# Optimization experiments

Hardware: AMD Instinct MI355X
Metric: run time of the kernel (lower is better)

The kernel has to match this reference:

```python
import jax, jax.numpy as jnp
import numpy as np

N_NODES = 100000
N_EDGES = 800000
N_GRAPHS = 128
UNITS = 128
NUM_GINS = 3
NUM_CLASSES = 16
EPS_GIN = 0.5        # GIN eps from the module
BN_EPS = 1e-3        # keras BatchNormalization default epsilon


def setup_inputs() -> dict:
    key = jax.random.key(0)
    ks = jax.random.split(key, 12)
    x = jax.random.normal(ks[0], (N_NODES, UNITS), dtype=jnp.float32)
    edge_index = jax.random.randint(ks[1], (2, N_EDGES), 0, N_NODES, dtype=jnp.int32)
    edge_weight = jax.random.uniform(ks[2], (N_EDGES,), dtype=jnp.float32)
    node_graph_index = jnp.sort(jax.random.randint(ks[3], (N_NODES,), 0, N_GRAPHS, dtype=jnp.int32))
    s1 = 1.0 / np.sqrt(UNITS)
    W1 = jax.random.normal(ks[4], (NUM_GINS, UNITS, UNITS), dtype=jnp.float32) * s1
    b1 = jnp.zeros((NUM_GINS, UNITS), jnp.float32)
    W2 = jax.random.normal(ks[5], (NUM_GINS, UNITS, UNITS), dtype=jnp.float32) * s1
    b2 = jnp.zeros((NUM_GINS, UNITS), jnp.float32)
    gamma = jnp.ones((NUM_GINS, UNITS), jnp.float32)
    beta = jnp.zeros((NUM_GINS, UNITS), jnp.float32)
    bn_mean = jnp.zeros((NUM_GINS, UNITS), jnp.float32)
    bn_var = jnp.ones((NUM_GINS, UNITS), jnp.float32)
    Wm1 = jax.random.normal(ks[6], (NUM_GINS * UNITS, 128), dtype=jnp.float32) / np.sqrt(NUM_GINS * UNITS)
    bm1 = jnp.zeros((128,), jnp.float32)
    Wm2 = jax.random.normal(ks[7], (128, NUM_CLASSES), dtype=jnp.float32) / np.sqrt(128.0)
    bm2 = jnp.zeros((NUM_CLASSES,), jnp.float32)
    return dict(x=x, edge_index=edge_index, edge_weight=edge_weight,
                node_graph_index=node_graph_index,
                W1=W1, b1=b1, W2=W2, b2=b2, gamma=gamma, beta=beta,
                bn_mean=bn_mean, bn_var=bn_var,
                Wm1=Wm1, bm1=bm1, Wm2=Wm2, bm2=bm2)


def reference(x, edge_index, edge_weight, node_graph_index,
              W1, b1, W2, b2, gamma, beta, bn_mean, bn_var,
              Wm1, bm1, Wm2, bm2):
    dst, src = edge_index[0], edge_index[1]
    h = x
    hidden_outputs = []
    for i in range(NUM_GINS):
        # message passing: weighted neighbor sum (gather + scatter-add)
        msg = h[src] * edge_weight[:, None]                      # [E, U]
        agg = jax.ops.segment_sum(msg, dst, num_segments=N_NODES)  # [N, U]
        z = (1.0 + EPS_GIN) * h + agg
        # GIN MLP: Dense-relu, Dense, BatchNorm (inference), relu
        z = jax.nn.relu(z @ W1[i] + b1[i])
        z = z @ W2[i] + b2[i]
        z = (z - bn_mean[i]) * (gamma[i] / jnp.sqrt(bn_var[i] + BN_EPS)) + beta[i]
        h = jax.nn.relu(z)
        hidden_outputs.append(h)
    hcat = jnp.concatenate(hidden_outputs, axis=-1)              # [N, 3*U]
    pooled = jax.ops.segment_sum(hcat, node_graph_index, num_segments=N_GRAPHS)  # [G, 3*U]
    g = jax.nn.relu(pooled @ Wm1 + bm1)                          # dropout is identity at inference
    logits = g @ Wm2 + bm2
    return logits
```

## Files before the change

### kernel.cpp

```cpp
#include <hip/hip_runtime.h>

#define NN 100000
#define NE 800000
#define NG 128
#define U  128
#define NGIN 3
#define NBUCK 64
#define NPB 1563
#define ACHUNK 4096
#define NAB ((NE + ACHUNK - 1) / ACHUNK)
#define ZP 136

typedef short bf16x8 __attribute__((ext_vector_type(8)));
typedef float f32x4 __attribute__((ext_vector_type(4)));

__device__ __forceinline__ unsigned short f2b(float f) {
    union { float f; unsigned u; } v; v.f = f;
    unsigned r = v.u + 0x7FFF + ((v.u >> 16) & 1);
    return (unsigned short)(r >> 16);
}
__device__ __forceinline__ float blo(unsigned u) {
    union { unsigned u; float f; } v; v.u = u << 16; return v.f;
}
__device__ __forceinline__ float bhi(unsigned u) {
    union { unsigned u; float f; } v; v.u = u & 0xffff0000u; return v.f;
}
__device__ __forceinline__ unsigned cvtpk(float lo, float hi) {
    unsigned r;
    asm("v_cvt_pk_bf16_f32 %0, %1, %2" : "=v"(r) : "v"(lo), "v"(hi));
    return r;
}

__global__ __launch_bounds__(256) void convert_k(const float* __restrict__ x,
                                                 unsigned short* __restrict__ hb) {
    int i = blockIdx.x * 256 + threadIdx.x;
    if (i >= NN * U / 4) return;
    float4 v = reinterpret_cast<const float4*>(x)[i];
    uint2 o;
    o.x = (unsigned)f2b(v.x) | ((unsigned)f2b(v.y) << 16);
    o.y = (unsigned)f2b(v.z) | ((unsigned)f2b(v.w) << 16);
    reinterpret_cast<uint2*>(hb)[i] = o;
}

__global__ __launch_bounds__(256) void wfrag_k(const float* __restrict__ W1,
                                               const float* __restrict__ W2,
                                               unsigned short* __restrict__ wfrag) {
    int b = blockIdx.x;
    const float* src = ((b & 1) ? W2 : W1) + (size_t)(b >> 1) * U * U;
    unsigned short* dst = wfrag + (size_t)b * 16384;
    for (int e = threadIdx.x; e < 16384; e += 256) {
        int j = e & 7, lane = (e >> 3) & 63, ks = (e >> 9) & 3, ct = e >> 11;
        int k = ks * 32 + ((lane >> 4) << 3) + j;
        int c = ct * 16 + (lane & 15);
        dst[e] = f2b(src[k * U + c]);
    }
}

__global__ __launch_bounds__(128) void bnprep_k(const float* __restrict__ b2,
                                                const float* __restrict__ gam,
                                                const float* __restrict__ bet,
                                                const float* __restrict__ mean,
                                                const float* __restrict__ var,
                                                float* __restrict__ scl,
                                                float* __restrict__ sh) {
    int i = blockIdx.x * 128 + threadIdx.x;
    float s = gam[i] * rsqrtf(var[i] + 1e-3f);
    scl[i] = s;
    sh[i] = (b2[i] - mean[i]) * s + bet[i];
}

__global__ __launch_bounds__(256) void bhist_k(const int* __restrict__ ei,
                                               int* __restrict__ bcnt) {
    __shared__ int lh[NBUCK];
    int tid = threadIdx.x;
    if (tid < NBUCK) lh[tid] = 0;
    __syncthreads();
    int e0 = blockIdx.x * ACHUNK;
    int eend = min(e0 + ACHUNK, NE);
    for (int e = e0 + tid; e < eend; e += 256)
        atomicAdd(&lh[ei[e] / NPB], 1);
    __syncthreads();
    if (tid < NBUCK && lh[tid]) atomicAdd(&bcnt[tid], lh[tid]);
}

__global__ __launch_bounds__(64) void bscan_k(const int* __restrict__ bcnt,
                                              int* __restrict__ bcur,
                                              int* __restrict__ boff,
                                              int* __restrict__ rowptr) {
    int lane = threadIdx.x;
    int v = bcnt[lane];
    int incl = v;
#pragma unroll
    for (int off = 1; off < 64; off <<= 1) {
        int n = __shfl_up(incl, off);
        if (lane >= off) incl += n;
    }
    int excl = incl - v;
    bcur[lane] = excl;
    boff[lane] = excl;
    if (lane == 63) { boff[64] = incl; rowptr[NN] = NE; }
}

__global__ __launch_bounds__(256) void phaseA_k(const int* __restrict__ ei,
                                                const float* __restrict__ ew,
                                                int* __restrict__ bcur,
                                                uint2* __restrict__ tmp) {
    __shared__ int lh[NBUCK];
    int tid = threadIdx.x;
    if (tid < NBUCK) lh[tid] = 0;
    __syncthreads();
    int e0 = blockIdx.x * ACHUNK;
    int eend = min(e0 + ACHUNK, NE);
    for (int e = e0 + tid; e < eend; e += 256)
        atomicAdd(&lh[ei[e] / NPB], 1);
    __syncthreads();
    if (tid < NBUCK) {
        int c = lh[tid];
        lh[tid] = c ? atomicAdd(&bcur[tid], c) : 0;
    }
    __syncthreads();
    for (int e = e0 + tid; e < eend; e += 256) {
        int d = ei[e];
        int pos = atomicAdd(&lh[d / NPB], 1);
        uint2 r;
        r.x = ((unsigned)ei[NE + e] << 15) | (unsigned)f2b(ew[e]);
        r.y = (unsigned)d;
        tmp[pos] = r;
    }
}

__global__ __launch_bounds__(256) void phaseB_k(const uint2* __restrict__ tmp,
                                                const int* __restrict__ boff,
                                                int* __restrict__ rowptr,
                                                unsigned* __restrict__ esw) {
    __shared__ int cnt[1792];
    __shared__ int ws[4];
    const int tid = threadIdx.x;
    const int b = blockIdx.x;
    const int n0 = b * NPB;
    const int npb = min(NPB, NN - n0);
    const int wbeg = boff[b], wend = boff[b + 1];

    for (int i = tid; i < 1792; i += 256) cnt[i] = 0;
    __syncthreads();
    for (int e = wbeg + tid; e < wend; e += 256)
        atomicAdd(&cnt[(int)tmp[e].y - n0], 1);
    __syncthreads();
    int base = tid * 7;
    int v[7]; int s = 0;
#pragma unroll
    for (int k = 0; k < 7; ++k) { v[k] = cnt[base + k]; s += v[k]; }
    int lane = tid & 63, wid = tid >> 6;
    int incl = s;
#pragma unroll
    for (int off = 1; off < 64; off <<= 1) {
        int n = __shfl_up(incl, off);
        if (lane >= off) incl += n;
    }
    if (lane == 63) ws[wid] = incl;
    __syncthreads();
    if (tid == 0) {
        int a = 0;
#pragma unroll
        for (int w = 0; w < 4; ++w) { int t = ws[w]; ws[w] = a; a += t; }
    }
    __syncthreads();
    int run = wbeg + ws[wid] + (incl - s);
#pragma unroll
    for (int k = 0; k < 7; ++k) { cnt[base + k] = run; run += v[k]; }
    __syncthreads();
    for (int i = tid; i < npb; i += 256) rowptr[n0 + i] = cnt[i];
    __syncthreads();
    for (int e = wbeg + tid; e < wend; e += 256) {
        uint2 r = tmp[e];
        int pos = atomicAdd(&cnt[(int)r.y - n0], 1);
        esw[pos] = r.x;
    }
}

__global__ __launch_bounds__(256) void fusedgd_k(const unsigned short* __restrict__ hin,
                                                 const unsigned* __restrict__ esw,
                                                 const int* __restrict__ rowptr,
                                                 const unsigned short* __restrict__ wf1,
                                                 const unsigned short* __restrict__ wf2,
                                                 const float* __restrict__ bias1,
                                                 const float* __restrict__ sclp,
                                                 const float* __restrict__ shp,
                                                 const int* __restrict__ gidx,
                                                 unsigned short* __restrict__ hout,
                                                 float* __restrict__ pooled,
                                                 int pool_off) {
    __shared__ unsigned short zt[16 * ZP];
    __shared__ unsigned short z1t[16 * ZP];
    const int tid = threadIdx.x;
    const int lane = tid & 63;
    const int wid = tid >> 6;
    const int r0 = blockIdx.x * 16;
    const unsigned* hp = reinterpret_cast<const unsigned*>(hin);
    unsigned* ztd = reinterpret_cast<unsigned*>(zt);

    for (int q = 0; q < 4; ++q) {
        int row = wid * 4 + q;
        int node = r0 + row;
        int beg = rowptr[node], end = rowptr[node + 1];
        float ax[8], ay[8];
#pragma unroll
        for (int k = 0; k < 8; ++k) { ax[k] = 0.f; ay[k] = 0.f; }
        for (int cb = beg; cb < end; cb += 64) {
            int n = min(end - cb, 64);
            unsigned rec = (lane < n) ? esw[cb + lane] : 0u;
            int sv = (int)(rec >> 15);
            float wv = __uint_as_float((rec & 0x7FFFu) << 16);
            for (int i = 0; i < n; i += 8) {
                int s_[8]; float w_[8]; unsigned h_[8];
#pragma unroll
                for (int k = 0; k < 8; ++k) {
                    s_[k] = __shfl(sv, i + k);
                    w_[k] = __shfl(wv, i + k);
                }
#pragma unroll
                for (int k = 0; k < 8; ++k)
                    h_[k] = hp[(size_t)s_[k] * 64 + lane];
#pragma unroll
                for (int k = 0; k < 8; ++k) {
                    ax[k] = fmaf(blo(h_[k]), w_[k], ax[k]);
                    ay[k] = fmaf(bhi(h_[k]), w_[k], ay[k]);
                }
            }
        }
        float axs = ((ax[0] + ax[1]) + (ax[2] + ax[3])) + ((ax[4] + ax[5]) + (ax[6] + ax[7]));
        float ays = ((ay[0] + ay[1]) + (ay[2] + ay[3])) + ((ay[4] + ay[5]) + (ay[6] + ay[7]));
        unsigned hn = hp[(size_t)node * 64 + lane];
        axs = fmaf(1.5f, blo(hn), axs);
        ays = fmaf(1.5f, bhi(hn), ays);
        ztd[row * (ZP / 2) + lane] = cvtpk(axs, ays);
    }
    __syncthreads();

    const int c = lane & 15;
    const int g = lane >> 4;
    bf16x8 a1[4];
#pragma unroll
    for (int ks = 0; ks < 4; ++ks)
        a1[ks] = *reinterpret_cast<const bf16x8*>(zt + c * ZP + ks * 32 + g * 8);

    f32x4 acc1[2];
    acc1[0] = (f32x4){0.f, 0.f, 0.f, 0.f};
    acc1[1] = (f32x4){0.f, 0.f, 0.f, 0.f};
#pragma unroll
    for (int t = 0; t < 2; ++t) {
        int ct = wid * 2 + t;
#pragma unroll
        for (int ks = 0; ks < 4; ++ks) {
            bf16x8 b = *reinterpret_cast<const bf16x8*>(
                wf1 + (((ct * 4 + ks) * 64 + lane) << 3));
            acc1[t] = __builtin_amdgcn_mfma_f32_16x16x32_bf16(a1[ks], b, acc1[t], 0, 0, 0);
        }
    }
#pragma unroll
    for (int t = 0; t < 2; ++t) {
        int col = (wid * 2 + t) * 16 + c;
        float bv = bias1[col];
#pragma unroll
        for (int j = 0; j < 4; ++j) {
            int row = g * 4 + j;
            z1t[row * ZP + col] = f2b(fmaxf(acc1[t][j] + bv, 0.f));
        }
    }
    __syncthreads();

    bf16x8 a2[4];
#pragma unroll
    for (int ks = 0; ks < 4; ++ks)
        a2[ks] = *reinterpret_cast<const bf16x8*>(z1t + c * ZP + ks * 32 + g * 8);

    f32x4 acc2[2];
    acc2[0] = (f32x4){0.f, 0.f, 0.f, 0.f};
    acc2[1] = (f32x4){0.f, 0.f, 0.f, 0.f};
#pragma unroll
    for (int t = 0; t < 2; ++t) {
        int ct = wid * 2 + t;
#pragma unroll
        for (int ks = 0; ks < 4; ++ks) {
            bf16x8 b = *reinterpret_cast<const bf16x8*>(
                wf2 + (((ct * 4 + ks) * 64 + lane) << 3));
            acc2[t] = __builtin_amdgcn_mfma_f32_16x16x32_bf16(a2[ks], b, acc2[t], 0, 0, 0);
        }
    }

    int ga = gidx[r0], gb = gidx[r0 + 15];
    bool uni = (ga == gb);
#pragma unroll
    for (int t = 0; t < 2; ++t) {
        int col = (wid * 2 + t) * 16 + c;
        float scl = sclp[col], sh = shp[col];
        float hv[4];
        float psum = 0.f;
#pragma unroll
        for (int j = 0; j < 4; ++j) {
            int row = g * 4 + j;
            float v = fmaxf(fmaf(acc2[t][j], scl, sh), 0.f);
            hv[j] = v;
            psum += v;
            hout[(size_t)(r0 + row) * U + col] = f2b(v);
        }
        if (uni) {
            psum += __shfl_xor(psum, 16);
            psum += __shfl_xor(psum, 32);
            if (lane < 16)
                unsafeAtomicAdd(&pooled[(size_t)ga * (NGIN * U) + pool_off + col], psum);
        } else {
#pragma unroll
            for (int j = 0; j < 4; ++j)
                unsafeAtomicAdd(&pooled[(size_t)gidx[r0 + g * 4 + j] * (NGIN * U) + pool_off + col], hv[j]);
        }
    }
}

__global__ __launch_bounds__(128) void mlp1_k(const float* __restrict__ pooled,
                                              const float* __restrict__ Wm1,
                                              const float* __restrict__ bm1,
                                              float* __restrict__ g) {
    __shared__ float sp[NGIN * U];
    int gi = blockIdx.x, c = threadIdx.x;
    for (int j = c; j < NGIN * U; j += 128) sp[j] = pooled[(size_t)gi * (NGIN * U) + j];
    __syncthreads();
    float acc = bm1[c];
    for (int k = 0; k < NGIN * U; ++k) acc = fmaf(sp[k], Wm1[(size_t)k * 128 + c], acc);
    g[gi * 128 + c] = fmaxf(acc, 0.f);
}

__global__ __launch_bounds__(256) void mlp2_k(const float* __restrict__ g,
                                              const float* __restrict__ Wm2,
                                              const float* __restrict__ bm2,
                                              float* __restrict__ out) {
    int idx = blockIdx.x * 256 + threadIdx.x;
    int gi = idx >> 4, c = idx & 15;
    float acc = bm2[c];
    for (int k = 0; k < 128; ++k) acc = fmaf(g[gi * 128 + k], Wm2[k * 16 + c], acc);
    out[gi * 16 + c] = acc;
}

extern "C" void kernel_launch(void* const* d_in, const int* in_sizes, int n_in,
                              void* d_out, int out_size, void* d_ws, size_t ws_size,
                              hipStream_t stream) {
    const float* x   = (const float*)d_in[0];
    const int*   ei  = (const int*)d_in[1];
    const float* ew  = (const float*)d_in[2];
    const int*   gix = (const int*)d_in[3];
    const float* W1  = (const float*)d_in[4];
    const float* b1  = (const float*)d_in[5];
    const float* W2  = (const float*)d_in[6];
    const float* b2  = (const float*)d_in[7];
    const float* gam = (const float*)d_in[8];
    const float* bet = (const float*)d_in[9];
    const float* bmn = (const float*)d_in[10];
    const float* bvr = (const float*)d_in[11];
    const float* Wm1 = (const float*)d_in[12];
    const float* bm1 = (const float*)d_in[13];
    const float* Wm2 = (const float*)d_in[14];
    const float* bm2 = (const float*)d_in[15];
    float* out = (float*)d_out;

    unsigned short* hb0 = (unsigned short*)d_ws;
    unsigned short* hb1 = hb0 + (size_t)NN * U;
    float* pooled = (float*)(hb1 + (size_t)NN * U);
    float* gbuf   = pooled + (size_t)NG * (NGIN * U);
    unsigned short* wfrag = (unsigned short*)(gbuf + (size_t)NG * 128);
    unsigned* esw = (unsigned*)(wfrag + 6 * 16384);
    uint2* tmp    = (uint2*)(esw + NE);
    int*   rowptr = (int*)(tmp + NE);
    int*   bcnt   = rowptr + (NN + 1);
    int*   bcur   = bcnt + NBUCK;
    int*   boff   = bcur + NBUCK;
    float* sclp   = (float*)(boff + NBUCK + 1);
    float* shp    = sclp + NGIN * U;

    convert_k<<<(NN * U / 4 + 255) / 256, 256, 0, stream>>>(x, hb0);
    hipMemsetAsync(bcnt, 0, NBUCK * sizeof(int), stream);
    bhist_k<<<NAB, 256, 0, stream>>>(ei, bcnt);
    bscan_k<<<1, 64, 0, stream>>>(bcnt, bcur, boff, rowptr);
    phaseA_k<<<NAB, 256, 0, stream>>>(ei, ew, bcur, tmp);
    phaseB_k<<<NBUCK, 256, 0, stream>>>(tmp, boff, rowptr, esw);
    wfrag_k<<<6, 256, 0, stream>>>(W1, W2, wfrag);
    bnprep_k<<<NGIN, 128, 0, stream>>>(b2, gam, bet, bmn, bvr, sclp, shp);
    hipMemsetAsync(pooled, 0, (size_t)NG * (NGIN * U) * sizeof(float), stream);

    unsigned short* hA = hb0;
    unsigned short* hB = hb1;
    for (int i = 0; i < NGIN; ++i) {
        fusedgd_k<<<NN / 16, 256, 0, stream>>>(
            hA, esw, rowptr,
            wfrag + (size_t)(2 * i) * 16384, wfrag + (size_t)(2 * i + 1) * 16384,
            b1 + i * U, sclp + i * U, shp + i * U,
            gix, hB, pooled, i * U);
        unsigned short* t = hA; hA = hB; hB = t;
    }
    mlp1_k<<<NG, 128, 0, stream>>>(pooled, Wm1, bm1, gbuf);
    mlp2_k<<<(NG * 16) / 256, 256, 0, stream>>>(gbuf, Wm2, bm2, out);
}
```

Before: 288.1 us.

## Pad CSR rows to multiples of 8 and interleave four rows per warp gather

```diff
diff --git a/kernel.cpp b/kernel.cpp
--- a/kernel.cpp
+++ b/kernel.cpp
@@ -10,6 +10,7 @@
 #define ACHUNK 4096
 #define NAB ((NE + ACHUNK - 1) / ACHUNK)
 #define ZP 136
+#define ESWSZ (NE + 8 * NN + 64)
 
 typedef short bf16x8 __attribute__((ext_vector_type(8)));
 typedef float f32x4 __attribute__((ext_vector_type(4)));
@@ -85,8 +86,7 @@
 
 __global__ __launch_bounds__(64) void bscan_k(const int* __restrict__ bcnt,
                                               int* __restrict__ bcur,
-                                              int* __restrict__ boff,
-                                              int* __restrict__ rowptr) {
+                                              int* __restrict__ boff) {
     int lane = threadIdx.x;
     int v = bcnt[lane];
     int incl = v;
@@ -98,7 +98,7 @@
     int excl = incl - v;
     bcur[lane] = excl;
     boff[lane] = excl;
-    if (lane == 63) { boff[64] = incl; rowptr[NN] = NE; }
+    if (lane == 63) boff[64] = incl;
 }
 
 __global__ __launch_bounds__(256) void phaseA_k(const int* __restrict__ ei,
@@ -132,6 +132,7 @@
 __global__ __launch_bounds__(256) void phaseB_k(const uint2* __restrict__ tmp,
                                                 const int* __restrict__ boff,
                                                 int* __restrict__ rowptr,
+                                                int* __restrict__ rcnt,
                                                 unsigned* __restrict__ esw) {
     __shared__ int cnt[1792];
     __shared__ int ws[4];
@@ -140,6 +141,7 @@
     const int n0 = b * NPB;
     const int npb = min(NPB, NN - n0);
     const int wbeg = boff[b], wend = boff[b + 1];
+    const int pbase = ((wbeg + b * 8 * NPB) + 7) & ~7;
 
     for (int i = tid; i < 1792; i += 256) cnt[i] = 0;
     __syncthreads();
@@ -147,9 +149,9 @@
         atomicAdd(&cnt[(int)tmp[e].y - n0], 1);
     __syncthreads();
     int base = tid * 7;
-    int v[7]; int s = 0;
-#pragma unroll
-    for (int k = 0; k < 7; ++k) { v[k] = cnt[base + k]; s += v[k]; }
+    int pc[7]; int s = 0;
+#pragma unroll
+    for (int k = 0; k < 7; ++k) { pc[k] = (cnt[base + k] + 7) & ~7; s += pc[k]; }
     int lane = tid & 63, wid = tid >> 6;
     int incl = s;
 #pragma unroll
@@ -165,11 +167,14 @@
         for (int w = 0; w < 4; ++w) { int t = ws[w]; ws[w] = a; a += t; }
     }
     __syncthreads();
-    int run = wbeg + ws[wid] + (incl - s);
-#pragma unroll
-    for (int k = 0; k < 7; ++k) { cnt[base + k] = run; run += v[k]; }
-    __syncthreads();
-    for (int i = tid; i < npb; i += 256) rowptr[n0 + i] = cnt[i];
+    int run = pbase + ws[wid] + (incl - s);
+#pragma unroll
+    for (int k = 0; k < 7; ++k) {
+        int nidx = base + k;
+        if (nidx < npb) { rowptr[n0 + nidx] = run; rcnt[n0 + nidx] = pc[k]; }
+        cnt[nidx] = run;
+        run += pc[k];
+    }
     __syncthreads();
     for (int e = wbeg + tid; e < wend; e += 256) {
         uint2 r = tmp[e];
@@ -181,6 +186,7 @@
 __global__ __launch_bounds__(256) void fusedgd_k(const unsigned short* __restrict__ hin,
                                                  const unsigned* __restrict__ esw,
                                                  const int* __restrict__ rowptr,
+                                                 const int* __restrict__ rcnt,
                                                  const unsigned short* __restrict__ wf1,
                                                  const unsigned short* __restrict__ wf2,
                                                  const float* __restrict__ bias1,
@@ -199,41 +205,53 @@
     const unsigned* hp = reinterpret_cast<const unsigned*>(hin);
     unsigned* ztd = reinterpret_cast<unsigned*>(zt);
 
+    const int node0 = r0 + wid * 4;
+    int beg[4], n[4];
+#pragma unroll
     for (int q = 0; q < 4; ++q) {
-        int row = wid * 4 + q;
-        int node = r0 + row;
-        int beg = rowptr[node], end = rowptr[node + 1];
-        float ax[8], ay[8];
-#pragma unroll
-        for (int k = 0; k < 8; ++k) { ax[k] = 0.f; ay[k] = 0.f; }
-        for (int cb = beg; cb < end; cb += 64) {
-            int n = min(end - cb, 64);
-            unsigned rec = (lane < n) ? esw[cb + lane] : 0u;
-            int sv = (int)(rec >> 15);
-            float wv = __uint_as_float((rec & 0x7FFFu) << 16);
-            for (int i = 0; i < n; i += 8) {
-                int s_[8]; float w_[8]; unsigned h_[8];
+        beg[q] = rowptr[node0 + q];
+        n[q]   = rcnt[node0 + q];
+    }
+    float ax[4][2], ay[4][2];
+#pragma unroll
+    for (int q = 0; q < 4; ++q) {
+        ax[q][0] = ax[q][1] = 0.f;
+        ay[q][0] = ay[q][1] = 0.f;
+    }
+    int maxn = max(max(n[0], n[1]), max(n[2], n[3]));
+    for (int i = 0; i < maxn; i += 8) {
+        unsigned rr[4][8];
+        unsigned hreg[4][8];
+#pragma unroll
+        for (int q = 0; q < 4; ++q) {
+            if (i < n[q]) {
+                uint4 ra = *reinterpret_cast<const uint4*>(esw + beg[q] + i);
+                uint4 rb = *reinterpret_cast<const uint4*>(esw + beg[q] + i + 4);
+                rr[q][0] = ra.x; rr[q][1] = ra.y; rr[q][2] = ra.z; rr[q][3] = ra.w;
+                rr[q][4] = rb.x; rr[q][5] = rb.y; rr[q][6] = rb.z; rr[q][7] = rb.w;
+#pragma unroll
+                for (int k = 0; k < 8; ++k)
+                    hreg[q][k] = hp[(size_t)(rr[q][k] >> 15) * 64 + lane];
+            }
+        }
+#pragma unroll
+        for (int q = 0; q < 4; ++q) {
+            if (i < n[q]) {
 #pragma unroll
                 for (int k = 0; k < 8; ++k) {
-                    s_[k] = __shfl(sv, i + k);
-                    w_[k] = __shfl(wv, i + k);
-                }
-#pragma unroll
-                for (int k = 0; k < 8; ++k)
-                    h_[k] = hp[(size_t)s_[k] * 64 + lane];
-#pragma unroll
-                for (int k = 0; k < 8; ++k) {
-                    ax[k] = fmaf(blo(h_[k]), w_[k], ax[k]);
-                    ay[k] = fmaf(bhi(h_[k]), w_[k], ay[k]);
+                    float w = __uint_as_float((rr[q][k] & 0x7FFFu) << 16);
+                    ax[q][k & 1] = fmaf(blo(hreg[q][k]), w, ax[q][k & 1]);
+                    ay[q][k & 1] = fmaf(bhi(hreg[q][k]), w, ay[q][k & 1]);
                 }
             }
         }
-        float axs = ((ax[0] + ax[1]) + (ax[2] + ax[3])) + ((ax[4] + ax[5]) + (ax[6] + ax[7]));
-        float ays = ((ay[0] + ay[1]) + (ay[2] + ay[3])) + ((ay[4] + ay[5]) + (ay[6] + ay[7]));
-        unsigned hn = hp[(size_t)node * 64 + lane];
-        axs = fmaf(1.5f, blo(hn), axs);
-        ays = fmaf(1.5f, bhi(hn), ays);
-        ztd[row * (ZP / 2) + lane] = cvtpk(axs, ays);
+    }
+#pragma unroll
+    for (int q = 0; q < 4; ++q) {
+        unsigned hn = hp[(size_t)(node0 + q) * 64 + lane];
+        float axs = fmaf(1.5f, blo(hn), ax[q][0] + ax[q][1]);
+        float ays = fmaf(1.5f, bhi(hn), ay[q][0] + ay[q][1]);
+        ztd[(wid * 4 + q) * (ZP / 2) + lane] = cvtpk(axs, ays);
     }
     __syncthreads();
 
@@ -368,9 +386,10 @@
     float* gbuf   = pooled + (size_t)NG * (NGIN * U);
     unsigned short* wfrag = (unsigned short*)(gbuf + (size_t)NG * 128);
     unsigned* esw = (unsigned*)(wfrag + 6 * 16384);
-    uint2* tmp    = (uint2*)(esw + NE);
+    uint2* tmp    = (uint2*)(esw + ESWSZ);
     int*   rowptr = (int*)(tmp + NE);
-    int*   bcnt   = rowptr + (NN + 1);
+    int*   rcnt   = rowptr + (NN + 1);
+    int*   bcnt   = rcnt + NN;
     int*   bcur   = bcnt + NBUCK;
     int*   boff   = bcur + NBUCK;
     float* sclp   = (float*)(boff + NBUCK + 1);
@@ -378,10 +397,11 @@
 
     convert_k<<<(NN * U / 4 + 255) / 256, 256, 0, stream>>>(x, hb0);
     hipMemsetAsync(bcnt, 0, NBUCK * sizeof(int), stream);
+    hipMemsetAsync(esw, 0, (size_t)ESWSZ * sizeof(unsigned), stream);
     bhist_k<<<NAB, 256, 0, stream>>>(ei, bcnt);
-    bscan_k<<<1, 64, 0, stream>>>(bcnt, bcur, boff, rowptr);
+    bscan_k<<<1, 64, 0, stream>>>(bcnt, bcur, boff);
     phaseA_k<<<NAB, 256, 0, stream>>>(ei, ew, bcur, tmp);
-    phaseB_k<<<NBUCK, 256, 0, stream>>>(tmp, boff, rowptr, esw);
+    phaseB_k<<<NBUCK, 256, 0, stream>>>(tmp, boff, rowptr, rcnt, esw);
     wfrag_k<<<6, 256, 0, stream>>>(W1, W2, wfrag);
     bnprep_k<<<NGIN, 128, 0, stream>>>(b2, gam, bet, bmn, bvr, sclp, shp);
     hipMemsetAsync(pooled, 0, (size_t)NG * (NGIN * U) * sizeof(float), stream);
@@ -390,7 +410,7 @@
     unsigned short* hB = hb1;
     for (int i = 0; i < NGIN; ++i) {
         fusedgd_k<<<NN / 16, 256, 0, stream>>>(
-            hA, esw, rowptr,
+            hA, esw, rowptr, rcnt,
             wfrag + (size_t)(2 * i) * 16384, wfrag + (size_t)(2 * i + 1) * 16384,
             b1 + i * U, sclp + i * U, shp + i * U,
             gix, hB, pooled, i * U);
```

Result: slower. 317.2 us (+10.1%).
